# Optimization experiments

Measured on AMD Instinct MI355X. Metric: run time of the kernel, lower is better.

## Reference

```python
import jax, jax.numpy as jnp
import numpy as np

D_MODEL = 2048
N_HEADS = 32
N_KV = 8
D_K = D_MODEL // N_HEADS  # 64
N_REP = N_HEADS // N_KV   # 4


def setup_inputs() -> dict:
    key = jax.random.key(0)
    ks = jax.random.split(key, 5)
    B, T = 2, 2048
    s = 0.02
    return {
        "x": jax.random.normal(ks[0], (B, T, D_MODEL), dtype=jnp.float32),
        "Wq": jax.random.normal(ks[1], (D_MODEL, D_MODEL), dtype=jnp.float32) * s,
        "Wk": jax.random.normal(ks[2], (N_KV * D_K, D_MODEL), dtype=jnp.float32) * s,
        "Wv": jax.random.normal(ks[3], (N_KV * D_K, D_MODEL), dtype=jnp.float32) * s,
        "Wo": jax.random.normal(ks[4], (D_MODEL, D_MODEL), dtype=jnp.float32) * s,
    }


def reference(x, Wq, Wk, Wv, Wo):
    B, T, C = x.shape
    # projections (torch Linear: x @ W.T)
    Q = (x @ Wq.T).reshape(B, T, N_KV, N_REP, D_K)  # group query heads by kv group
    K = (x @ Wk.T).reshape(B, T, N_KV, D_K)
    V = (x @ Wv.T).reshape(B, T, N_KV, D_K)
    scale = 1.0 / jnp.sqrt(jnp.asarray(D_K, dtype=x.dtype))
    # scores: (B, n_kv, n_rep, T, T) == repeated-KV scores without materializing repeats
    scores = jnp.einsum('btgrd,bsgd->bgrts', Q, K) * scale
    causal_mask = jnp.triu(jnp.ones((T, T), dtype=bool), k=1)
    scores = jnp.where(causal_mask, -jnp.inf, scores)
    attn = jax.nn.softmax(scores, axis=-1)
    out = jnp.einsum('bgrts,bsgd->btgrd', attn, V).reshape(B, T, C)
    return out @ Wo.T
```

## Files before the change

kernel.cpp:

```cpp
#include <hip/hip_runtime.h>
#include <hip/hip_bf16.h>

typedef __attribute__((ext_vector_type(8))) short bf16x8;
typedef __attribute__((ext_vector_type(4))) float floatx4;

constexpr int D_MODEL = 2048;
constexpr int N_HEADS = 32;
constexpr int N_KV    = 8;
constexpr int B_      = 2;
constexpr int T_      = 2048;
constexpr int BT      = B_ * T_;
constexpr int NQKV    = 3072;

constexpr float Q_SCALE = 0.18033688011112042f;

__device__ __forceinline__ unsigned short f2bf(float f) {
    __hip_bfloat16 h = __float2bfloat16(f);
    return *reinterpret_cast<unsigned short*>(&h);
}

__device__ __forceinline__ unsigned bfpack_rn(float a, float b) {
    unsigned ba = __builtin_bit_cast(unsigned, a);
    unsigned bb = __builtin_bit_cast(unsigned, b);
    return ((ba + 0x8000u) >> 16) | ((bb + 0x8000u) & 0xFFFF0000u);
}

__device__ __forceinline__ void gll16(const void* g, void* l) {
    typedef const __attribute__((address_space(1))) unsigned int* gp_t;
    typedef __attribute__((address_space(3))) unsigned int* lp_t;
    __builtin_amdgcn_global_load_lds((gp_t)g, (lp_t)l, 16, 0, 0);
}

__global__ __launch_bounds__(256) void cvt_all(
        const float* __restrict__ x,  const float* __restrict__ wq,
        const float* __restrict__ wk, const float* __restrict__ wv,
        unsigned short* __restrict__ dst) {
    size_t i4 = (size_t)blockIdx.x * 256 + threadIdx.x;
    size_t e = i4 * 4;
    const float* src; size_t off;
    if (e < 8388608)        { src = x;  off = 0; }
    else if (e < 12582912)  { src = wq; off = 8388608; }
    else if (e < 13631488)  { src = wk; off = 12582912; }
    else                    { src = wv; off = 13631488; }
    float4 f = *reinterpret_cast<const float4*>(src + (e - off));
    unsigned short u[4] = {f2bf(f.x), f2bf(f.y), f2bf(f.z), f2bf(f.w)};
    reinterpret_cast<uint2*>(dst)[i4] = *reinterpret_cast<const uint2*>(u);
}

__global__ __launch_bounds__(256) void cvt_bf16(
        const float* __restrict__ src, unsigned short* __restrict__ dst, int n4) {
    int i = blockIdx.x * 256 + threadIdx.x;
    if (i < n4) {
        float4 f = reinterpret_cast<const float4*>(src)[i];
        unsigned short u[4] = {f2bf(f.x), f2bf(f.y), f2bf(f.z), f2bf(f.w)};
        reinterpret_cast<uint2*>(dst)[i] = *reinterpret_cast<const uint2*>(u);
    }
}

template<bool C_F32, bool SCALEQ, bool FUSEV>
__global__ __launch_bounds__(256) void gemm128(
        const unsigned short* __restrict__ A,
        const unsigned short* __restrict__ Bb,
        void* __restrict__ Cp,
        unsigned short* __restrict__ Vtp,
        int M, int N, int K) {
    __shared__ unsigned short As[128 * 64];
    __shared__ unsigned short Bs[128 * 64];
    const int t = threadIdx.x;
    const int wave = t >> 6, lane = t & 63;
    const int l16 = lane & 15, quad = lane >> 4;
    const int wm = (wave & 1) * 64, wn = (wave >> 1) * 64;

    const int gx = gridDim.x;
    int bid = blockIdx.y * gx + blockIdx.x;
    const int cpx = (gx * gridDim.y) >> 3;
    bid = (bid & 7) * cpx + (bid >> 3);
    const int mtile = (bid / gx) * 128, ntile = (bid % gx) * 128;

    floatx4 acc[4][4] = {};

    for (int k0 = 0; k0 < K; k0 += 64) {
        __syncthreads();
#pragma unroll
        for (int c = 0; c < 4; c++) {
            int s = (c * 4 + wave) * 64 + lane;
            int row = s >> 3, k8 = (s & 7) ^ (row & 7);
            gll16(&A[(size_t)(mtile + row) * K + k0 + k8 * 8], &As[(c * 4 + wave) * 512]);
            gll16(&Bb[(size_t)(ntile + row) * K + k0 + k8 * 8], &Bs[(c * 4 + wave) * 512]);
        }
        __syncthreads();
#pragma unroll
        for (int kc = 0; kc < 2; kc++) {
            bf16x8 af[4], bfr[4];
#pragma unroll
            for (int i = 0; i < 4; i++) {
                int arow = wm + i * 16 + l16;
                af[i] = *reinterpret_cast<const bf16x8*>(
                    &As[(arow * 8 + ((kc * 4 + quad) ^ (arow & 7))) * 8]);
                int brow = wn + i * 16 + l16;
                bfr[i] = *reinterpret_cast<const bf16x8*>(
                    &Bs[(brow * 8 + ((kc * 4 + quad) ^ (brow & 7))) * 8]);
            }
#pragma unroll
            for (int i = 0; i < 4; i++)
#pragma unroll
                for (int jn = 0; jn < 4; jn++)
                    acc[i][jn] = __builtin_amdgcn_mfma_f32_16x16x32_bf16(
                        af[i], bfr[jn], acc[i][jn], 0, 0, 0);
        }
    }
    float cscale = (SCALEQ && ntile < 2048) ? Q_SCALE : 1.0f;
#pragma unroll
    for (int i = 0; i < 4; i++)
#pragma unroll
        for (int jn = 0; jn < 4; jn++) {
            int col = ntile + wn + jn * 16 + l16;
#pragma unroll
            for (int r = 0; r < 4; r++) {
                int row = mtile + wm + i * 16 + quad * 4 + r;
                if constexpr (C_F32) {
                    ((float*)Cp)[(size_t)row * N + col] = acc[i][jn][r];
                } else {
                    unsigned short v = f2bf(acc[i][jn][r] * cscale);
                    ((unsigned short*)Cp)[(size_t)row * N + col] = v;
                    if constexpr (FUSEV)
                        if (col >= 2560) {
                            int d = col - 2560;
                            int gg = d >> 6, dd = d & 63;
                            int bb = row >> 11, tok = row & 2047;
                            Vtp[(((size_t)bb * 8 + gg) * 64 + dd) * T_ + tok] = v;
                        }
                }
            }
        }
}

__global__ __launch_bounds__(512, 4) void attn8(
        const unsigned short* __restrict__ QKV,
        const unsigned short* __restrict__ Vt,
        unsigned short* __restrict__ O) {
    __shared__ unsigned short Ks[2][64 * 64];
    __shared__ unsigned short Vs[2][64 * 64];
    __shared__ unsigned short Ps[8][16 * 72];
    const int j  = blockIdx.x;
    const int bh = blockIdx.y;
    const int b = bh >> 5, h = bh & 31;
    const int g = h >> 2;
    const int t = threadIdx.x, wave = t >> 6, lane = t & 63;
    const int l16 = lane & 15, quad = lane >> 4;

    bf16x8 ones;
#pragma unroll
    for (int i = 0; i < 8; i++) ones[i] = (short)0x3F80;

    const int srow = t >> 3;
    const int sk8  = (t & 7) ^ (srow & 7);
    const unsigned short* kbase =
        QKV + (size_t)(b * T_ + srow) * NQKV + 2048 + g * 64 + sk8 * 8;
    const unsigned short* vbase =
        Vt + ((size_t)(b * 8 + g) * 64 + srow) * T_ + sk8 * 8;
    unsigned short* kdst0 = &Ks[0][wave * 512];
    unsigned short* vdst0 = &Vs[0][wave * 512];
    unsigned short* kdst1 = &Ks[1][wave * 512];
    unsigned short* vdst1 = &Vs[1][wave * 512];

    for (int pp = 0; pp < 2; pp++) {
        const int qtl = pp ? (15 - j) : j;
        const int q0  = qtl * 128;
        const int qlo = q0 + wave * 16;

        const unsigned short* qptr =
            QKV + (size_t)(b * T_ + qlo + l16) * NQKV + h * 64;
        bf16x8 qf0 = *reinterpret_cast<const bf16x8*>(qptr + quad * 8);
        bf16x8 qf1 = *reinterpret_cast<const bf16x8*>(qptr + 32 + quad * 8);

        floatx4 o[4] = {};
        floatx4 lacc = {};

        const unsigned short* kp = kbase;
        const unsigned short* vp = vbase;

        const int nit = qtl + 1;
        for (int it = 0; it < nit; it++) {
            __syncthreads();
            gll16(kp, kdst0);
            gll16(vp, vdst0);
            gll16(kp + 64 * NQKV, kdst1);
            gll16(vp + 64, vdst1);
            kp += 128 * NQKV;
            vp += 128;
            __syncthreads();

#pragma unroll
            for (int u = 0; u < 2; u++) {
                const int kb = (it * 2 + u) * 64;
                if (kb > qlo + 15) continue;
                const bool needmask = (kb + 63 > qlo);

#pragma unroll
                for (int km = 0; km < 4; km++) {
                    int krow = km * 16 + l16;
                    bf16x8 k0 = *reinterpret_cast<const bf16x8*>(
                        &Ks[u][(krow * 8 + (quad ^ (krow & 7))) * 8]);
                    bf16x8 k1 = *reinterpret_cast<const bf16x8*>(
                        &Ks[u][(krow * 8 + ((4 + quad) ^ (krow & 7))) * 8]);
                    floatx4 z = {};
                    __builtin_amdgcn_s_setprio(1);
                    z = __builtin_amdgcn_mfma_f32_16x16x32_bf16(k0, qf0, z, 0, 0, 0);
                    z = __builtin_amdgcn_mfma_f32_16x16x32_bf16(k1, qf1, z, 0, 0, 0);
                    __builtin_amdgcn_s_setprio(0);
                    float p[4];
#pragma unroll
                    for (int r = 0; r < 4; r++)
                        p[r] = __builtin_amdgcn_exp2f(z[r]);
                    if (needmask) {
                        int qq = qlo + l16;
#pragma unroll
                        for (int r = 0; r < 4; r++)
                            if ((kb + km * 16 + quad * 4 + r) > qq) p[r] = 0.f;
                    }
                    uint2 w;
                    w.x = bfpack_rn(p[0], p[1]);
                    w.y = bfpack_rn(p[2], p[3]);
                    *reinterpret_cast<uint2*>(
                        &Ps[wave][l16 * 72 + km * 16 + quad * 4]) = w;
                }

                bf16x8 pf[2];
                __builtin_amdgcn_s_setprio(1);
#pragma unroll
                for (int ks = 0; ks < 2; ks++)
                    pf[ks] = *reinterpret_cast<const bf16x8*>(
                        &Ps[wave][l16 * 72 + ks * 32 + quad * 8]);
                lacc = __builtin_amdgcn_mfma_f32_16x16x32_bf16(pf[0], ones, lacc, 0, 0, 0);
                lacc = __builtin_amdgcn_mfma_f32_16x16x32_bf16(pf[1], ones, lacc, 0, 0, 0);
#pragma unroll
                for (int dt = 0; dt < 4; dt++) {
                    int vrow = dt * 16 + l16;
                    bf16x8 v0 = *reinterpret_cast<const bf16x8*>(
                        &Vs[u][(vrow * 8 + (quad ^ (vrow & 7))) * 8]);
                    bf16x8 v1 = *reinterpret_cast<const bf16x8*>(
                        &Vs[u][(vrow * 8 + ((4 + quad) ^ (vrow & 7))) * 8]);
                    o[dt] = __builtin_amdgcn_mfma_f32_16x16x32_bf16(pf[0], v0, o[dt], 0, 0, 0);
                    o[dt] = __builtin_amdgcn_mfma_f32_16x16x32_bf16(pf[1], v1, o[dt], 0, 0, 0);
                }
                __builtin_amdgcn_s_setprio(0);
            }
        }

#pragma unroll
        for (int r = 0; r < 4; r++) {
            float inv = 1.0f / lacc[r];
            int row = b * T_ + qlo + quad * 4 + r;
#pragma unroll
            for (int dt = 0; dt < 4; dt++)
                O[(size_t)row * D_MODEL + h * 64 + dt * 16 + l16] =
                    f2bf(o[dt][r] * inv);
        }
    }
}

extern "C" void kernel_launch(void* const* d_in, const int* in_sizes, int n_in,
                              void* d_out, int out_size, void* d_ws, size_t ws_size,
                              hipStream_t stream) {
    const float* x  = (const float*)d_in[0];
    const float* Wq = (const float*)d_in[1];
    const float* Wk = (const float*)d_in[2];
    const float* Wv = (const float*)d_in[3];
    const float* Wo = (const float*)d_in[4];

    unsigned short* xb   = (unsigned short*)d_ws;
    unsigned short* Wqkv = xb + (size_t)BT * D_MODEL;
    unsigned short* QKVo = Wqkv + (size_t)NQKV * D_MODEL;
    unsigned short* Vt   = QKVo + (size_t)BT * NQKV;
    unsigned short* Aw   = xb;
    unsigned short* Wob  = Wqkv;

    dim3 blk(256);
    cvt_all<<<dim3(14336), blk, 0, stream>>>(x, Wq, Wk, Wv, xb);
    gemm128<false, true, true><<<dim3(NQKV / 128, BT / 128), blk, 0, stream>>>(
        xb, Wqkv, QKVo, Vt, BT, NQKV, D_MODEL);
    cvt_bf16<<<dim3(D_MODEL * D_MODEL / 4 / 256), blk, 0, stream>>>(
        Wo, Wob, D_MODEL * D_MODEL / 4);
    attn8<<<dim3(8, B_ * N_HEADS), dim3(512), 0, stream>>>(QKVo, Vt, Aw);
    gemm128<true, false, false><<<dim3(D_MODEL / 128, BT / 128), blk, 0, stream>>>(
        Aw, Wob, d_out, nullptr, BT, D_MODEL, D_MODEL);
}
```

Baseline: 280.6 us.

## Replace QKV projection GEMM with 256x256 double-buffered ping-pong pipelined kernel

Adds a new 512-thread GEMM with 256x256 output tiles, double-buffered LDS staged through direct global-to-LDS loads, and an XOR swizzle. Each K step is split into phases that interleave staging loads with MFMA clusters, using explicit barriers, waitcnts and setprio. The QKV projection uses this kernel, aiming for more data reuse and overlap of memory with compute. The cost is a grid of only 192 blocks, which may underfill the CUs, plus much higher register and LDS use per block.

Measured after the change: 299.8 us. +6.9%, slower.

```diff
diff --git a/kernel.cpp b/kernel.cpp
--- a/kernel.cpp
+++ b/kernel.cpp
@@ -57,12 +57,181 @@
     }
 }
 
-template<bool C_F32, bool SCALEQ, bool FUSEV>
+#define PH_PRE  asm volatile("" ::: "memory");                      \
+                __builtin_amdgcn_s_barrier();                       \
+                asm volatile("" ::: "memory")
+#define PH_POST asm volatile("s_waitcnt lgkmcnt(0)" ::: "memory");  \
+                __builtin_amdgcn_sched_barrier(0);                  \
+                __builtin_amdgcn_s_barrier();                       \
+                asm volatile("" ::: "memory")
+#define QUAD(m0, A00, A01, A10, A11)                                          \
+    __builtin_amdgcn_s_setprio(1);                                            \
+    _Pragma("unroll")                                                         \
+    for (int nf = 0; nf < 4; nf++) {                                          \
+        acc[m0][nf] = __builtin_amdgcn_mfma_f32_16x16x32_bf16(                \
+            A00, bfr[nf][0], acc[m0][nf], 0, 0, 0);                           \
+        acc[m0][nf] = __builtin_amdgcn_mfma_f32_16x16x32_bf16(                \
+            A01, bfr[nf][1], acc[m0][nf], 0, 0, 0);                           \
+        acc[m0 + 1][nf] = __builtin_amdgcn_mfma_f32_16x16x32_bf16(            \
+            A10, bfr[nf][0], acc[m0 + 1][nf], 0, 0, 0);                       \
+        acc[m0 + 1][nf] = __builtin_amdgcn_mfma_f32_16x16x32_bf16(            \
+            A11, bfr[nf][1], acc[m0 + 1][nf], 0, 0, 0);                       \
+    }                                                                         \
+    __builtin_amdgcn_s_setprio(0)
+
+template<bool SCALEQ, bool FUSEV>
+__global__ __launch_bounds__(512, 2) void gemm256p(
+        const unsigned short* __restrict__ A,
+        const unsigned short* __restrict__ Bb,
+        unsigned short* __restrict__ Cp,
+        unsigned short* __restrict__ Vtp,
+        int M, int N, int K) {
+    __shared__ unsigned short As[2][2][128 * 64];
+    __shared__ unsigned short Bs[2][2][128 * 64];
+    const int t = threadIdx.x;
+    const int wave = t >> 6, lane = t & 63;
+    const int l16 = lane & 15, quad = lane >> 4;
+    const int wm  = wave & 1;
+    const int wn  = (wave >> 1) * 64;
+    const int bhf = wn >> 7;
+    const int bro = wn & 64;
+
+    const int gx = gridDim.x;
+    int bid = blockIdx.y * gx + blockIdx.x;
+    const int cpx = (gx * gridDim.y) >> 3;
+    bid = (bid & 7) * cpx + (bid >> 3);
+    const int mtile = (bid / gx) * 256, ntile = (bid % gx) * 256;
+
+    const int sr0 = t >> 3, sr1 = 64 + sr0;
+    const int sk0 = (t & 7) ^ (sr0 & 7), sk1 = (t & 7) ^ (sr1 & 7);
+
+    auto stageA = [&](int kt, int half, int d) {
+        const unsigned short* base = A + (size_t)(mtile + half * 128) * K + kt * 64;
+        gll16(base + (size_t)sr0 * K + sk0 * 8, &As[d][half][wave * 512]);
+        gll16(base + (size_t)sr1 * K + sk1 * 8, &As[d][half][(8 + wave) * 512]);
+    };
+    auto stageB = [&](int kt, int half, int d) {
+        const unsigned short* base = Bb + (size_t)(ntile + half * 128) * K + kt * 64;
+        gll16(base + (size_t)sr0 * K + sk0 * 8, &Bs[d][half][wave * 512]);
+        gll16(base + (size_t)sr1 * K + sk1 * 8, &Bs[d][half][(8 + wave) * 512]);
+    };
+    auto rdA = [&](int d, int mf, int kc) -> bf16x8 {
+        int r = mf * 16 + l16;
+        return *reinterpret_cast<const bf16x8*>(
+            &As[d][wm][(r * 8 + ((kc * 4 + quad) ^ (r & 7))) * 8]);
+    };
+    auto rdB = [&](int d, int nf, int kc) -> bf16x8 {
+        int r = bro + nf * 16 + l16;
+        return *reinterpret_cast<const bf16x8*>(
+            &Bs[d][bhf][(r * 8 + ((kc * 4 + quad) ^ (r & 7))) * 8]);
+    };
+
+    floatx4 acc[8][4] = {};
+    const int NKT = K >> 6;
+    const int NI  = NKT >> 1;
+
+    stageB(0, 0, 0); stageB(0, 1, 0);
+    stageA(0, 0, 0); stageA(0, 1, 0);
+    stageB(1, 0, 1); stageB(1, 1, 1);
+    asm volatile("s_waitcnt vmcnt(4)" ::: "memory");
+    PH_PRE;
+
+    for (int i = 0; i < NI; ++i) {
+        const bool nl = (i + 1 < NI);
+        const int k2 = 2 * i;
+        bf16x8 bfr[4][2];
+
+        {
+#pragma unroll
+            for (int nf = 0; nf < 4; nf++) {
+                bfr[nf][0] = rdB(0, nf, 0); bfr[nf][1] = rdB(0, nf, 1);
+            }
+            bf16x8 a00 = rdA(0, 0, 0), a01 = rdA(0, 0, 1);
+            bf16x8 a10 = rdA(0, 1, 0), a11 = rdA(0, 1, 1);
+            stageA(k2 + 1, 0, 1);
+            PH_PRE; QUAD(0, a00, a01, a10, a11); PH_POST;
+        }
+        {
+            bf16x8 a00 = rdA(0, 2, 0), a01 = rdA(0, 2, 1);
+            bf16x8 a10 = rdA(0, 3, 0), a11 = rdA(0, 3, 1);
+            stageA(k2 + 1, 1, 1);
+            PH_PRE; QUAD(2, a00, a01, a10, a11); PH_POST;
+        }
+        {
+            bf16x8 a00 = rdA(0, 4, 0), a01 = rdA(0, 4, 1);
+            bf16x8 a10 = rdA(0, 5, 0), a11 = rdA(0, 5, 1);
+            if (nl) stageB(k2 + 2, 0, 0);
+            PH_PRE; QUAD(4, a00, a01, a10, a11); PH_POST;
+        }
+        {
+            bf16x8 a00 = rdA(0, 6, 0), a01 = rdA(0, 6, 1);
+            bf16x8 a10 = rdA(0, 7, 0), a11 = rdA(0, 7, 1);
+            if (nl) {
+                stageB(k2 + 2, 1, 0);
+                asm volatile("s_waitcnt vmcnt(4)" ::: "memory");
+            } else {
+                asm volatile("s_waitcnt vmcnt(0)" ::: "memory");
+            }
+            PH_PRE; QUAD(6, a00, a01, a10, a11); PH_POST;
+        }
+        {
+#pragma unroll
+            for (int nf = 0; nf < 4; nf++) {
+                bfr[nf][0] = rdB(1, nf, 0); bfr[nf][1] = rdB(1, nf, 1);
+            }
+            bf16x8 a00 = rdA(1, 0, 0), a01 = rdA(1, 0, 1);
+            bf16x8 a10 = rdA(1, 1, 0), a11 = rdA(1, 1, 1);
+            if (nl) stageA(k2 + 2, 0, 0);
+            PH_PRE; QUAD(0, a00, a01, a10, a11); PH_POST;
+        }
+        {
+            bf16x8 a00 = rdA(1, 2, 0), a01 = rdA(1, 2, 1);
+            bf16x8 a10 = rdA(1, 3, 0), a11 = rdA(1, 3, 1);
+            if (nl) stageA(k2 + 2, 1, 0);
+            PH_PRE; QUAD(2, a00, a01, a10, a11); PH_POST;
+        }
+        {
+            bf16x8 a00 = rdA(1, 4, 0), a01 = rdA(1, 4, 1);
+            bf16x8 a10 = rdA(1, 5, 0), a11 = rdA(1, 5, 1);
+            if (nl) stageB(k2 + 3, 0, 1);
+            PH_PRE; QUAD(4, a00, a01, a10, a11); PH_POST;
+        }
+        {
+            bf16x8 a00 = rdA(1, 6, 0), a01 = rdA(1, 6, 1);
+            bf16x8 a10 = rdA(1, 7, 0), a11 = rdA(1, 7, 1);
+            if (nl) stageB(k2 + 3, 1, 1);
+            asm volatile("s_waitcnt vmcnt(4)" ::: "memory");
+            PH_PRE; QUAD(6, a00, a01, a10, a11); PH_POST;
+        }
+    }
+
+    float cscale = (SCALEQ && ntile < 2048) ? Q_SCALE : 1.0f;
+#pragma unroll
+    for (int i = 0; i < 8; i++)
+#pragma unroll
+        for (int jn = 0; jn < 4; jn++) {
+            int col = ntile + wn + jn * 16 + l16;
+#pragma unroll
+            for (int r = 0; r < 4; r++) {
+                int row = mtile + wm * 128 + i * 16 + quad * 4 + r;
+                unsigned short v = f2bf(acc[i][jn][r] * cscale);
+                Cp[(size_t)row * N + col] = v;
+                if constexpr (FUSEV)
+                    if (col >= 2560) {
+                        int d = col - 2560;
+                        int gg = d >> 6, dd = d & 63;
+                        int bb = row >> 11, tok = row & 2047;
+                        Vtp[(((size_t)bb * 8 + gg) * 64 + dd) * T_ + tok] = v;
+                    }
+            }
+        }
+}
+
+template<bool C_F32, bool SCALEQ>
 __global__ __launch_bounds__(256) void gemm128(
         const unsigned short* __restrict__ A,
         const unsigned short* __restrict__ Bb,
         void* __restrict__ Cp,
-        unsigned short* __restrict__ Vtp,
         int M, int N, int K) {
     __shared__ unsigned short As[128 * 64];
     __shared__ unsigned short Bs[128 * 64];
@@ -118,19 +287,11 @@
 #pragma unroll
             for (int r = 0; r < 4; r++) {
                 int row = mtile + wm + i * 16 + quad * 4 + r;
-                if constexpr (C_F32) {
+                if constexpr (C_F32)
                     ((float*)Cp)[(size_t)row * N + col] = acc[i][jn][r];
-                } else {
-                    unsigned short v = f2bf(acc[i][jn][r] * cscale);
-                    ((unsigned short*)Cp)[(size_t)row * N + col] = v;
-                    if constexpr (FUSEV)
-                        if (col >= 2560) {
-                            int d = col - 2560;
-                            int gg = d >> 6, dd = d & 63;
-                            int bb = row >> 11, tok = row & 2047;
-                            Vtp[(((size_t)bb * 8 + gg) * 64 + dd) * T_ + tok] = v;
-                        }
-                }
+                else
+                    ((unsigned short*)Cp)[(size_t)row * N + col] =
+                        f2bf(acc[i][jn][r] * cscale);
             }
         }
 }
@@ -278,11 +439,11 @@
 
     dim3 blk(256);
     cvt_all<<<dim3(14336), blk, 0, stream>>>(x, Wq, Wk, Wv, xb);
-    gemm128<false, true, true><<<dim3(NQKV / 128, BT / 128), blk, 0, stream>>>(
+    gemm256p<true, true><<<dim3(NQKV / 256, BT / 256), dim3(512), 0, stream>>>(
         xb, Wqkv, QKVo, Vt, BT, NQKV, D_MODEL);
     cvt_bf16<<<dim3(D_MODEL * D_MODEL / 4 / 256), blk, 0, stream>>>(
         Wo, Wob, D_MODEL * D_MODEL / 4);
     attn8<<<dim3(8, B_ * N_HEADS), dim3(512), 0, stream>>>(QKVo, Vt, Aw);
-    gemm128<true, false, false><<<dim3(D_MODEL / 128, BT / 128), blk, 0, stream>>>(
-        Aw, Wob, d_out, nullptr, BT, D_MODEL, D_MODEL);
-}
+    gemm128<true, false><<<dim3(D_MODEL / 128, BT / 128), blk, 0, stream>>>(
+        Aw, Wob, d_out, BT, D_MODEL, D_MODEL);
+}
```

## Share K/V tile loads across both paired query tiles in attention

Applied to the files above, without the earlier changes.

The attention kernel previously processed its two paired query tiles (j and 15-j) one after the other, reloading K/V tiles from global memory for each. Now both tiles' Q fragments and accumulators stay live, and a single pass over K/V tiles (up to the longer causal range) feeds both, so the shorter tile's K/V loads and syncs are no longer repeated. In exchange, register pressure roughly doubles for the accumulators and Q fragments under the 512x4 launch bound, which risks spills or lower occupancy.

After: 275.2 us (median of 2 runs). Within noise of the previous version (-1.9%).

```diff
diff --git a/kernel.cpp b/kernel.cpp
--- a/kernel.cpp
+++ b/kernel.cpp
@@ -135,7 +135,7 @@
         }
 }
 
-__global__ __launch_bounds__(512, 4) void attn8(
+__global__ __launch_bounds__(512, 4) void attn9(
         const unsigned short* __restrict__ QKV,
         const unsigned short* __restrict__ Vt,
         unsigned short* __restrict__ O) {
@@ -155,107 +155,116 @@
 
     const int srow = t >> 3;
     const int sk8  = (t & 7) ^ (srow & 7);
-    const unsigned short* kbase =
+    const unsigned short* kp =
         QKV + (size_t)(b * T_ + srow) * NQKV + 2048 + g * 64 + sk8 * 8;
-    const unsigned short* vbase =
+    const unsigned short* vp =
         Vt + ((size_t)(b * 8 + g) * 64 + srow) * T_ + sk8 * 8;
     unsigned short* kdst0 = &Ks[0][wave * 512];
     unsigned short* vdst0 = &Vs[0][wave * 512];
     unsigned short* kdst1 = &Ks[1][wave * 512];
     unsigned short* vdst1 = &Vs[1][wave * 512];
 
-    for (int pp = 0; pp < 2; pp++) {
-        const int qtl = pp ? (15 - j) : j;
-        const int q0  = qtl * 128;
-        const int qlo = q0 + wave * 16;
-
-        const unsigned short* qptr =
-            QKV + (size_t)(b * T_ + qlo + l16) * NQKV + h * 64;
-        bf16x8 qf0 = *reinterpret_cast<const bf16x8*>(qptr + quad * 8);
-        bf16x8 qf1 = *reinterpret_cast<const bf16x8*>(qptr + 32 + quad * 8);
-
-        floatx4 o[4] = {};
-        floatx4 lacc = {};
-
-        const unsigned short* kp = kbase;
-        const unsigned short* vp = vbase;
-
-        const int nit = qtl + 1;
-        for (int it = 0; it < nit; it++) {
-            __syncthreads();
-            gll16(kp, kdst0);
-            gll16(vp, vdst0);
-            gll16(kp + 64 * NQKV, kdst1);
-            gll16(vp + 64, vdst1);
-            kp += 128 * NQKV;
-            vp += 128;
-            __syncthreads();
-
-#pragma unroll
-            for (int u = 0; u < 2; u++) {
-                const int kb = (it * 2 + u) * 64;
-                if (kb > qlo + 15) continue;
-                const bool needmask = (kb + 63 > qlo);
-
-#pragma unroll
-                for (int km = 0; km < 4; km++) {
-                    int krow = km * 16 + l16;
-                    bf16x8 k0 = *reinterpret_cast<const bf16x8*>(
-                        &Ks[u][(krow * 8 + (quad ^ (krow & 7))) * 8]);
-                    bf16x8 k1 = *reinterpret_cast<const bf16x8*>(
-                        &Ks[u][(krow * 8 + ((4 + quad) ^ (krow & 7))) * 8]);
-                    floatx4 z = {};
-                    __builtin_amdgcn_s_setprio(1);
-                    z = __builtin_amdgcn_mfma_f32_16x16x32_bf16(k0, qf0, z, 0, 0, 0);
-                    z = __builtin_amdgcn_mfma_f32_16x16x32_bf16(k1, qf1, z, 0, 0, 0);
-                    __builtin_amdgcn_s_setprio(0);
-                    float p[4];
-#pragma unroll
-                    for (int r = 0; r < 4; r++)
-                        p[r] = __builtin_amdgcn_exp2f(z[r]);
-                    if (needmask) {
-                        int qq = qlo + l16;
-#pragma unroll
-                        for (int r = 0; r < 4; r++)
-                            if ((kb + km * 16 + quad * 4 + r) > qq) p[r] = 0.f;
-                    }
-                    uint2 w;
-                    w.x = bfpack_rn(p[0], p[1]);
-                    w.y = bfpack_rn(p[2], p[3]);
-                    *reinterpret_cast<uint2*>(
-                        &Ps[wave][l16 * 72 + km * 16 + quad * 4]) = w;
-                }
-
-                bf16x8 pf[2];
-                __builtin_amdgcn_s_setprio(1);
-#pragma unroll
-                for (int ks = 0; ks < 2; ks++)
-                    pf[ks] = *reinterpret_cast<const bf16x8*>(
-                        &Ps[wave][l16 * 72 + ks * 32 + quad * 8]);
-                lacc = __builtin_amdgcn_mfma_f32_16x16x32_bf16(pf[0], ones, lacc, 0, 0, 0);
-                lacc = __builtin_amdgcn_mfma_f32_16x16x32_bf16(pf[1], ones, lacc, 0, 0, 0);
-#pragma unroll
-                for (int dt = 0; dt < 4; dt++) {
-                    int vrow = dt * 16 + l16;
-                    bf16x8 v0 = *reinterpret_cast<const bf16x8*>(
-                        &Vs[u][(vrow * 8 + (quad ^ (vrow & 7))) * 8]);
-                    bf16x8 v1 = *reinterpret_cast<const bf16x8*>(
-                        &Vs[u][(vrow * 8 + ((4 + quad) ^ (vrow & 7))) * 8]);
-                    o[dt] = __builtin_amdgcn_mfma_f32_16x16x32_bf16(pf[0], v0, o[dt], 0, 0, 0);
-                    o[dt] = __builtin_amdgcn_mfma_f32_16x16x32_bf16(pf[1], v1, o[dt], 0, 0, 0);
-                }
-                __builtin_amdgcn_s_setprio(0);
+    const int qloA = j * 128 + wave * 16;
+    const int qloB = (15 - j) * 128 + wave * 16;
+
+    const unsigned short* qpA =
+        QKV + (size_t)(b * T_ + qloA + l16) * NQKV + h * 64;
+    const unsigned short* qpB =
+        QKV + (size_t)(b * T_ + qloB + l16) * NQKV + h * 64;
+    bf16x8 qfA0 = *reinterpret_cast<const bf16x8*>(qpA + quad * 8);
+    bf16x8 qfA1 = *reinterpret_cast<const bf16x8*>(qpA + 32 + quad * 8);
+    bf16x8 qfB0 = *reinterpret_cast<const bf16x8*>(qpB + quad * 8);
+    bf16x8 qfB1 = *reinterpret_cast<const bf16x8*>(qpB + 32 + quad * 8);
+
+    floatx4 oA[4] = {}, oB[4] = {};
+    floatx4 laccA = {}, laccB = {};
+
+    auto proc = [&](int u, int kb, int qlo, bf16x8 q0, bf16x8 q1,
+                    floatx4 (&o)[4], floatx4& lacc) {
+        if (kb > qlo + 15) return;
+        const bool needmask = (kb + 63 > qlo);
+
+#pragma unroll
+        for (int km = 0; km < 4; km++) {
+            int krow = km * 16 + l16;
+            bf16x8 k0 = *reinterpret_cast<const bf16x8*>(
+                &Ks[u][(krow * 8 + (quad ^ (krow & 7))) * 8]);
+            bf16x8 k1 = *reinterpret_cast<const bf16x8*>(
+                &Ks[u][(krow * 8 + ((4 + quad) ^ (krow & 7))) * 8]);
+            floatx4 z = {};
+            __builtin_amdgcn_s_setprio(1);
+            z = __builtin_amdgcn_mfma_f32_16x16x32_bf16(k0, q0, z, 0, 0, 0);
+            z = __builtin_amdgcn_mfma_f32_16x16x32_bf16(k1, q1, z, 0, 0, 0);
+            __builtin_amdgcn_s_setprio(0);
+            float p[4];
+#pragma unroll
+            for (int r = 0; r < 4; r++)
+                p[r] = __builtin_amdgcn_exp2f(z[r]);
+            if (needmask) {
+                int qq = qlo + l16;
+#pragma unroll
+                for (int r = 0; r < 4; r++)
+                    if ((kb + km * 16 + quad * 4 + r) > qq) p[r] = 0.f;
             }
-        }
-
-#pragma unroll
-        for (int r = 0; r < 4; r++) {
-            float inv = 1.0f / lacc[r];
-            int row = b * T_ + qlo + quad * 4 + r;
-#pragma unroll
-            for (int dt = 0; dt < 4; dt++)
-                O[(size_t)row * D_MODEL + h * 64 + dt * 16 + l16] =
-                    f2bf(o[dt][r] * inv);
+            uint2 w;
+            w.x = bfpack_rn(p[0], p[1]);
+            w.y = bfpack_rn(p[2], p[3]);
+            *reinterpret_cast<uint2*>(
+                &Ps[wave][l16 * 72 + km * 16 + quad * 4]) = w;
+        }
+
+        bf16x8 pf[2];
+        __builtin_amdgcn_s_setprio(1);
+#pragma unroll
+        for (int ks = 0; ks < 2; ks++)
+            pf[ks] = *reinterpret_cast<const bf16x8*>(
+                &Ps[wave][l16 * 72 + ks * 32 + quad * 8]);
+        lacc = __builtin_amdgcn_mfma_f32_16x16x32_bf16(pf[0], ones, lacc, 0, 0, 0);
+        lacc = __builtin_amdgcn_mfma_f32_16x16x32_bf16(pf[1], ones, lacc, 0, 0, 0);
+#pragma unroll
+        for (int dt = 0; dt < 4; dt++) {
+            int vrow = dt * 16 + l16;
+            bf16x8 v0 = *reinterpret_cast<const bf16x8*>(
+                &Vs[u][(vrow * 8 + (quad ^ (vrow & 7))) * 8]);
+            bf16x8 v1 = *reinterpret_cast<const bf16x8*>(
+                &Vs[u][(vrow * 8 + ((4 + quad) ^ (vrow & 7))) * 8]);
+            o[dt] = __builtin_amdgcn_mfma_f32_16x16x32_bf16(pf[0], v0, o[dt], 0, 0, 0);
+            o[dt] = __builtin_amdgcn_mfma_f32_16x16x32_bf16(pf[1], v1, o[dt], 0, 0, 0);
+        }
+        __builtin_amdgcn_s_setprio(0);
+    };
+
+    const int nit = 16 - j;
+    for (int it = 0; it < nit; it++) {
+        __syncthreads();
+        gll16(kp, kdst0);
+        gll16(vp, vdst0);
+        gll16(kp + 64 * NQKV, kdst1);
+        gll16(vp + 64, vdst1);
+        kp += 128 * NQKV;
+        vp += 128;
+        __syncthreads();
+
+#pragma unroll
+        for (int u = 0; u < 2; u++) {
+            const int kb = (it * 2 + u) * 64;
+            proc(u, kb, qloA, qfA0, qfA1, oA, laccA);
+            proc(u, kb, qloB, qfB0, qfB1, oB, laccB);
+        }
+    }
+
+#pragma unroll
+    for (int r = 0; r < 4; r++) {
+        float invA = 1.0f / laccA[r];
+        float invB = 1.0f / laccB[r];
+        int rowA = b * T_ + qloA + quad * 4 + r;
+        int rowB = b * T_ + qloB + quad * 4 + r;
+#pragma unroll
+        for (int dt = 0; dt < 4; dt++) {
+            O[(size_t)rowA * D_MODEL + h * 64 + dt * 16 + l16] =
+                f2bf(oA[dt][r] * invA);
+            O[(size_t)rowB * D_MODEL + h * 64 + dt * 16 + l16] =
+                f2bf(oB[dt][r] * invB);
         }
     }
 }
@@ -282,7 +291,7 @@
         xb, Wqkv, QKVo, Vt, BT, NQKV, D_MODEL);
     cvt_bf16<<<dim3(D_MODEL * D_MODEL / 4 / 256), blk, 0, stream>>>(
         Wo, Wob, D_MODEL * D_MODEL / 4);
-    attn8<<<dim3(8, B_ * N_HEADS), dim3(512), 0, stream>>>(QKVo, Vt, Aw);
+    attn9<<<dim3(8, B_ * N_HEADS), dim3(512), 0, stream>>>(QKVo, Vt, Aw);
     gemm128<true, false, false><<<dim3(D_MODEL / 128, BT / 128), blk, 0, stream>>>(
         Aw, Wob, d_out, nullptr, BT, D_MODEL, D_MODEL);
 }
```
